# Kernel tuning notes

Measured on AMD Instinct MI355X. Metric: run time of the kernel, lower is better.

## Reference

```python
import jax, jax.numpy as jnp
import numpy as np

N_HOPS = 2
DIM = 64
N_REL = 17          # n_relations; groups G = N_REL - 1 = 16
N_MEM = 32
BATCH = 1024
N_ENT = 100000      # entity table has N_ENT + 1 rows
KGE_W = 0.01
L2_W = 1e-5


def setup_inputs() -> dict:
    key = jax.random.key(0)
    ks = jax.random.split(key, 10)
    G = N_REL - 1
    pos_items = jax.random.randint(ks[0], (BATCH,), 0, N_ENT + 1)
    neg_items = jax.random.randint(ks[1], (BATCH,), 0, N_ENT + 1)
    memories_h = jax.random.randint(ks[2], (N_HOPS, BATCH, G, N_MEM), 0, N_ENT + 1)
    memories_r = jax.random.randint(ks[3], (N_HOPS, BATCH, G, N_MEM), 0, N_REL)
    memories_t = jax.random.randint(ks[4], (N_HOPS, BATCH, G, N_MEM), 0, N_ENT + 1)
    # xavier-ish scales
    entity_emb = jax.random.normal(ks[5], (N_ENT + 1, DIM), jnp.float32) * 0.1
    relation_emb = jax.random.normal(ks[6], (N_REL, DIM), jnp.float32) * 0.1
    transform_matrix = jax.random.normal(ks[7], (DIM, DIM), jnp.float32) * 0.2
    attn_w1 = jax.random.normal(ks[8], (N_HOPS, DIM, DIM), jnp.float32) * 0.2
    attn_w2 = jax.random.normal(ks[9], (N_HOPS, DIM), jnp.float32) * 0.2
    return dict(pos_items=pos_items, neg_items=neg_items,
                memories_h=memories_h, memories_r=memories_r, memories_t=memories_t,
                entity_emb=entity_emb, relation_emb=relation_emb,
                transform_matrix=transform_matrix, attn_w1=attn_w1, attn_w2=attn_w2)


def reference(pos_items, neg_items, memories_h, memories_r, memories_t,
              entity_emb, relation_emb, transform_matrix, attn_w1, attn_w2):
    G = N_REL - 1
    items_emb = entity_emb[pos_items]          # [B, D] (v, fixed across hops as in source)
    neg_emb = entity_emb[neg_items]            # [B, D]

    o_list = []
    items_emb_new = items_emb
    kge = jnp.float32(0.0)
    l2 = jnp.float32(0.0)
    for hop in range(N_HOPS):
        h = entity_emb[memories_h[hop]]        # [B, G, M, D]
        r = relation_emb[memories_r[hop]]      # [B, G, M, D]
        t = entity_emb[memories_t[hop]]        # [B, G, M, D]

        # Rh @ v with Rh = h r^T collapses to h * (r . v)  (identical math, no [D,D] tensors)
        rv = jnp.einsum('bgmd,bd->bgm', r, items_emb)           # [B, G, M]
        probs = (h * rv[..., None]).reshape(-1, N_MEM)          # faithful row-major reshape (mixes m,d as in source)
        probs = jax.nn.softmax(probs, axis=-1)
        probs = probs.reshape(BATCH * G, N_MEM, DIM)
        o = jnp.sum(t.reshape(BATCH * G, N_MEM, DIM) * probs, axis=1)  # [B*G, D]
        o = o.reshape(BATCH, G, DIM)

        # attention layer: Linear(D,D) -> Dropout(eval: identity) -> Linear(D,1) -> ReLU
        hid = jnp.einsum('bgd,de->bge', o, attn_w1[hop])
        a = jax.nn.relu(jnp.einsum('bge,e->bg', hid, attn_w2[hop]))
        w = jax.nn.softmax(a, axis=-1)                          # [B, G]
        o_h = jnp.sum(o * w[..., None], axis=1)                 # [B, D]

        items_emb_new = (items_emb + o_h) @ transform_matrix    # note: v stays the ORIGINAL items_emb
        o_list.append(o_h)

        # kge: hRt = h * (r . t), then mean(sigmoid(.))
        rt = jnp.einsum('bgmd,bgmd->bgm', r, t)
        kge = kge + jnp.mean(jax.nn.sigmoid(h * rt[..., None]))
        # l2: mean(sum(x*x)) over whole tensor == sum(x*x)
        l2 = l2 + jnp.sum(h * h) + jnp.sum(t * t) + jnp.sum(r * r)

    y = o_list[0]
    for i in range(1, N_HOPS):
        y = y + o_list[i]
    scores = jnp.sum(items_emb_new * y, axis=-1)
    neg_scores = jnp.sum(neg_emb * y, axis=-1)
    mf_loss = -jnp.mean(jax.nn.log_sigmoid(scores - neg_scores))
    return mf_loss - KGE_W * kge + L2_W * l2
```

## Files before the change

### kernel.cpp

```cpp
#include <hip/hip_runtime.h>


#define BATCH 1024
#define G     16
#define NMEM  32
#define DIM   64
#define NREL  17

template<int CTRL>
__device__ __forceinline__ float dpp_add(float x) {
    int y = __builtin_amdgcn_update_dpp(0, __float_as_int(x), CTRL, 0xF, 0xF, true);
    return x + __int_as_float(y);
}
template<int OFF>
__device__ __forceinline__ float swz_add(float x) {
    int y = __builtin_amdgcn_ds_swizzle(__float_as_int(x), OFF);
    return x + __int_as_float(y);
}
__device__ __forceinline__ float bperm(int byteidx, float x) {
    return __int_as_float(__builtin_amdgcn_ds_bpermute(byteidx, __float_as_int(x)));
}
__device__ __forceinline__ float red32(float v) {
    v = dpp_add<0xB1>(v);
    v = dpp_add<0x4E>(v);
    v = dpp_add<0x124>(v);
    v = dpp_add<0x128>(v);
    v = swz_add<0x401F>(v);
    return v;
}

__global__ void kgan_prep(const float* __restrict__ attn_w1,
                          const float* __restrict__ attn_w2,
                          float* __restrict__ u, double* __restrict__ acc) {
    int t = threadIdx.x;
    if (t < 4) acc[t] = 0.0;
    int hop = t >> 6, d = t & 63;
    float s = 0.f;
#pragma unroll
    for (int e = 0; e < DIM; ++e)
        s = fmaf(attn_w1[(hop * DIM + d) * DIM + e], attn_w2[hop * DIM + e], s);
    u[t] = s;
}

__launch_bounds__(1024, 8)
__global__ void kgan_main(const int* __restrict__ pos_items,
                          const int* __restrict__ neg_items,
                          const int* __restrict__ mem_h,
                          const int* __restrict__ mem_r,
                          const int* __restrict__ mem_t,
                          const float* __restrict__ ent,
                          const float* __restrict__ rel,
                          const float* __restrict__ Tm,
                          const float* __restrict__ u,
                          double* __restrict__ acc) {
    const int b    = blockIdx.x;
    const int tid  = threadIdx.x;
    const int lane = tid & 63;
    const int g    = tid >> 6;
    const int gU   = __builtin_amdgcn_readfirstlane(g);
    const int x32  = (lane ^ 32) << 2;

    __shared__ float  rel_lds[NREL][DIM];
    __shared__ float2 rv_rs[NREL];
    __shared__ float  a_lds[G];
    __shared__ float  o_lds[G][DIM];
    __shared__ float  red_k[G];
    __shared__ float  red_l[G];
    __shared__ float  y_lds[DIM];

    for (int i = tid; i < NREL * DIM; i += 1024)
        ((float*)rel_lds)[i] = rel[i];
    const float v = ent[(size_t)pos_items[b] * DIM + lane];
    __syncthreads();

    for (int rr = gU; rr < NREL; rr += G) {
        float rd = rel_lds[rr][lane];
        float s1 = red32(rd * v); s1 += bperm(x32, s1);
        float s2 = red32(rd * rd); s2 += bperm(x32, s2);
        if (lane == 0) rv_rs[rr] = make_float2(s1, s2);
    }
    __syncthreads();

    float kge_acc = 0.f, l2_acc = 0.f, l2r_acc = 0.f;
    float y0 = 0.f;
    float x1 = 0.f;

    for (int hop = 0; hop < 2; ++hop) {
        const int base = ((hop * BATCH + b) * G + gU) * NMEM;
        float o_d = 0.f;
#pragma unroll 4
        for (int m = 0; m < NMEM; ++m) {
            const int ih = mem_h[base + m];
            const int it = mem_t[base + m];
            const int ir = mem_r[base + m];
            const float  h   = ent[(size_t)ih * DIM + lane];
            const float  t   = ent[(size_t)it * DIM + lane];
            const float  r   = rel_lds[ir][lane];
            const float2 rr2 = rv_rs[ir];

            float e = __expf(h * rr2.x);
            float p = r * t;
            float de = e, dp = p;
            de = dpp_add<0xB1>(de);   dp = dpp_add<0xB1>(dp);
            de = dpp_add<0x4E>(de);   dp = dpp_add<0x4E>(dp);
            de = dpp_add<0x124>(de);  dp = dpp_add<0x124>(dp);
            de = dpp_add<0x128>(de);  dp = dpp_add<0x128>(dp);
            de = swz_add<0x401F>(de); dp = swz_add<0x401F>(dp);
            const float rt = dp + bperm(x32, dp);

            o_d = fmaf(t, e * __builtin_amdgcn_rcpf(de), o_d);

            const float z = h * rt;
            kge_acc += __builtin_amdgcn_rcpf(1.f + __expf(-z));

            l2_acc  = fmaf(h, h, l2_acc);
            l2_acc  = fmaf(t, t, l2_acc);
            l2r_acc += rr2.y;
        }

        float a = red32(o_d * u[hop * DIM + lane]);
        a += bperm(x32, a);
        a = fmaxf(a, 0.f);
        if (lane == 0) a_lds[g] = a;
        o_lds[g][lane] = o_d;
        __syncthreads();

        if (g == 0) {
            float amax = -1e30f;
#pragma unroll
            for (int gg = 0; gg < G; ++gg) amax = fmaxf(amax, a_lds[gg]);
            float wexp[G]; float wsum = 0.f;
#pragma unroll
            for (int gg = 0; gg < G; ++gg) { wexp[gg] = __expf(a_lds[gg] - amax); wsum += wexp[gg]; }
            float inv = 1.f / wsum;
            float oh = 0.f;
#pragma unroll
            for (int gg = 0; gg < G; ++gg) oh = fmaf(o_lds[gg][lane], wexp[gg] * inv, oh);
            y0 += oh;
            if (hop == 1) x1 = v + oh;
        }
        __syncthreads();
    }

    float kk = red32(kge_acc); kk += bperm(x32, kk);
    float ll = red32(l2_acc);  ll += bperm(x32, ll);
    if (lane == 0) { red_k[g] = kk; red_l[g] = ll + l2r_acc; }
    if (g == 0) y_lds[lane] = y0;
    __syncthreads();

    if (tid == 0) {
        float sk = 0.f, sl = 0.f;
#pragma unroll
        for (int gg = 0; gg < G; ++gg) { sk += red_k[gg]; sl += red_l[gg]; }
        atomicAdd(&acc[1], (double)sk);
        atomicAdd(&acc[2], (double)sl);
    }

    if (g == 0) {
        float z = 0.f;
#pragma unroll
        for (int e = 0; e < DIM; ++e) z = fmaf(Tm[lane * DIM + e], y_lds[e], z);
        float score = red32(x1 * z);  score  += bperm(x32, score);
        float nv    = ent[(size_t)neg_items[b] * DIM + lane];
        float nsc   = red32(nv * y0); nsc    += bperm(x32, nsc);
        if (lane == 0) {
            float diff = score - nsc;
            float ls = fminf(diff, 0.f) - log1pf(__expf(-fabsf(diff)));
            atomicAdd(&acc[0], (double)ls);
        }
    }
}

__global__ void kgan_finalize(const double* __restrict__ acc, float* __restrict__ out) {
    double mf  = -acc[0] / (double)BATCH;
    double kge = acc[1] / ((double)BATCH * G * NMEM * DIM);
    double l2  = acc[2];
    out[0] = (float)(mf - 0.01 * kge + 1e-5 * l2);
}

extern "C" void kernel_launch(void* const* d_in, const int* in_sizes, int n_in,
                              void* d_out, int out_size, void* d_ws, size_t ws_size,
                              hipStream_t stream) {
    const int*   pos_items = (const int*)d_in[0];
    const int*   neg_items = (const int*)d_in[1];
    const int*   mem_h     = (const int*)d_in[2];
    const int*   mem_r     = (const int*)d_in[3];
    const int*   mem_t     = (const int*)d_in[4];
    const float* ent       = (const float*)d_in[5];
    const float* rel       = (const float*)d_in[6];
    const float* Tm        = (const float*)d_in[7];
    const float* attn_w1   = (const float*)d_in[8];
    const float* attn_w2   = (const float*)d_in[9];

    double* acc = (double*)d_ws;
    float*  u   = (float*)((char*)d_ws + 64);

    kgan_prep<<<1, 128, 0, stream>>>(attn_w1, attn_w2, u, acc);
    kgan_main<<<BATCH, 1024, 0, stream>>>(pos_items, neg_items, mem_h, mem_r, mem_t,
                                          ent, rel, Tm, u, acc);
    kgan_finalize<<<1, 1, 0, stream>>>(acc, (float*)d_out);
}
```

Measured before the change: 162.8 us.

## Process two groups per wave with software-prefetched gathers and permlane-swap reductions

Halves the block to 512 threads so each wave handles two relation groups. Index and entity-row loads are prefetched two memories ahead in double buffers to hide gather latency. Cross-lane reductions now use the gfx950 permlane16/permlane32 swap instructions instead of ds_swizzle and ds_bpermute, which avoids LDS-path traffic. The cost is higher register pressure from the prefetch buffers, which may reduce occupancy.

```diff
diff --git a/kernel.cpp b/kernel.cpp
--- a/kernel.cpp
+++ b/kernel.cpp
@@ -12,21 +12,20 @@
     int y = __builtin_amdgcn_update_dpp(0, __float_as_int(x), CTRL, 0xF, 0xF, true);
     return x + __int_as_float(y);
 }
-template<int OFF>
-__device__ __forceinline__ float swz_add(float x) {
-    int y = __builtin_amdgcn_ds_swizzle(__float_as_int(x), OFF);
-    return x + __int_as_float(y);
-}
-__device__ __forceinline__ float bperm(int byteidx, float x) {
-    return __int_as_float(__builtin_amdgcn_ds_bpermute(byteidx, __float_as_int(x)));
-}
-__device__ __forceinline__ float red32(float v) {
+__device__ __forceinline__ float red32p(float v) {
     v = dpp_add<0xB1>(v);
     v = dpp_add<0x4E>(v);
     v = dpp_add<0x124>(v);
     v = dpp_add<0x128>(v);
-    v = swz_add<0x401F>(v);
-    return v;
+    float a = v, b = v;
+    asm("v_permlane16_swap_b32 %0, %1" : "+v"(a), "+v"(b));
+    return a + b;
+}
+__device__ __forceinline__ float red64p(float v) {
+    v = red32p(v);
+    float a = v, b = v;
+    asm("v_permlane32_swap_b32 %0, %1" : "+v"(a), "+v"(b));
+    return a + b;
 }
 
 __global__ void kgan_prep(const float* __restrict__ attn_w1,
@@ -42,7 +41,38 @@
     u[t] = s;
 }
 
-__launch_bounds__(1024, 8)
+#define PREF(IH, IT, IR, HV, TV, M0)                                     \
+    _Pragma("unroll") for (int grp = 0; grp < 2; ++grp) {                \
+        _Pragma("unroll") for (int j = 0; j < 2; ++j) {                  \
+            IH[grp][j] = mem_h[base[grp] + (M0) + j];                    \
+            IT[grp][j] = mem_t[base[grp] + (M0) + j];                    \
+            IR[grp][j] = mem_r[base[grp] + (M0) + j];                    \
+            HV[grp][j] = ent[(size_t)IH[grp][j] * DIM + lane];           \
+            TV[grp][j] = ent[(size_t)IT[grp][j] * DIM + lane];           \
+        }                                                                \
+    }
+
+#define COMP(IR, HV, TV)                                                 \
+    _Pragma("unroll") for (int grp = 0; grp < 2; ++grp) {                \
+        _Pragma("unroll") for (int j = 0; j < 2; ++j) {                  \
+            const int    ir  = IR[grp][j];                               \
+            const float  h   = HV[grp][j];                               \
+            const float  t   = TV[grp][j];                               \
+            const float2 rr2 = rv_rs[ir];                                \
+            const float  r   = rel_lds[ir][lane];                        \
+            float e  = __expf(h * rr2.x);                                \
+            float de = red32p(e);                                        \
+            float rt = red64p(r * t);                                    \
+            o_d[grp] = fmaf(t, e * __builtin_amdgcn_rcpf(de), o_d[grp]); \
+            float z  = h * rt;                                           \
+            kge_acc += __builtin_amdgcn_rcpf(1.f + __expf(-z));          \
+            l2_acc   = fmaf(h, h, l2_acc);                               \
+            l2_acc   = fmaf(t, t, l2_acc);                               \
+            l2r_acc += rr2.y;                                            \
+        }                                                                \
+    }
+
+__launch_bounds__(512, 8)
 __global__ void kgan_main(const int* __restrict__ pos_items,
                           const int* __restrict__ neg_items,
                           const int* __restrict__ mem_h,
@@ -56,27 +86,27 @@
     const int b    = blockIdx.x;
     const int tid  = threadIdx.x;
     const int lane = tid & 63;
-    const int g    = tid >> 6;
-    const int gU   = __builtin_amdgcn_readfirstlane(g);
-    const int x32  = (lane ^ 32) << 2;
+    const int wid  = __builtin_amdgcn_readfirstlane(tid >> 6);
+    const int g0   = wid;
+    const int g1   = wid + 8;
 
     __shared__ float  rel_lds[NREL][DIM];
     __shared__ float2 rv_rs[NREL];
     __shared__ float  a_lds[G];
     __shared__ float  o_lds[G][DIM];
-    __shared__ float  red_k[G];
-    __shared__ float  red_l[G];
+    __shared__ float  red_k[8];
+    __shared__ float  red_l[8];
     __shared__ float  y_lds[DIM];
 
-    for (int i = tid; i < NREL * DIM; i += 1024)
+    for (int i = tid; i < NREL * DIM; i += 512)
         ((float*)rel_lds)[i] = rel[i];
     const float v = ent[(size_t)pos_items[b] * DIM + lane];
     __syncthreads();
 
-    for (int rr = gU; rr < NREL; rr += G) {
+    for (int rr = wid; rr < NREL; rr += 8) {
         float rd = rel_lds[rr][lane];
-        float s1 = red32(rd * v); s1 += bperm(x32, s1);
-        float s2 = red32(rd * rd); s2 += bperm(x32, s2);
+        float s1 = red64p(rd * v);
+        float s2 = red64p(rd * rd);
         if (lane == 0) rv_rs[rr] = make_float2(s1, s2);
     }
     __syncthreads();
@@ -85,47 +115,36 @@
     float y0 = 0.f;
     float x1 = 0.f;
 
+#pragma unroll 1
     for (int hop = 0; hop < 2; ++hop) {
-        const int base = ((hop * BATCH + b) * G + gU) * NMEM;
-        float o_d = 0.f;
-#pragma unroll 4
-        for (int m = 0; m < NMEM; ++m) {
-            const int ih = mem_h[base + m];
-            const int it = mem_t[base + m];
-            const int ir = mem_r[base + m];
-            const float  h   = ent[(size_t)ih * DIM + lane];
-            const float  t   = ent[(size_t)it * DIM + lane];
-            const float  r   = rel_lds[ir][lane];
-            const float2 rr2 = rv_rs[ir];
-
-            float e = __expf(h * rr2.x);
-            float p = r * t;
-            float de = e, dp = p;
-            de = dpp_add<0xB1>(de);   dp = dpp_add<0xB1>(dp);
-            de = dpp_add<0x4E>(de);   dp = dpp_add<0x4E>(dp);
-            de = dpp_add<0x124>(de);  dp = dpp_add<0x124>(dp);
-            de = dpp_add<0x128>(de);  dp = dpp_add<0x128>(dp);
-            de = swz_add<0x401F>(de); dp = swz_add<0x401F>(dp);
-            const float rt = dp + bperm(x32, dp);
-
-            o_d = fmaf(t, e * __builtin_amdgcn_rcpf(de), o_d);
-
-            const float z = h * rt;
-            kge_acc += __builtin_amdgcn_rcpf(1.f + __expf(-z));
-
-            l2_acc  = fmaf(h, h, l2_acc);
-            l2_acc  = fmaf(t, t, l2_acc);
-            l2r_acc += rr2.y;
+        int base[2];
+        base[0] = ((hop * BATCH + b) * G + g0) * NMEM;
+        base[1] = base[0] + 8 * NMEM;
+
+        float o_d[2] = {0.f, 0.f};
+        int   ih0[2][2], it0[2][2], ir0[2][2];
+        int   ih1[2][2], it1[2][2], ir1[2][2];
+        float hv0[2][2], tv0[2][2], hv1[2][2], tv1[2][2];
+
+        PREF(ih0, it0, ir0, hv0, tv0, 0);
+#pragma unroll 1
+        for (int mbp = 0; mbp < 8; ++mbp) {
+            const int m1 = mbp * 4 + 2;
+            PREF(ih1, it1, ir1, hv1, tv1, m1);
+            COMP(ir0, hv0, tv0);
+            if (mbp < 7) { PREF(ih0, it0, ir0, hv0, tv0, m1 + 2); }
+            COMP(ir1, hv1, tv1);
         }
 
-        float a = red32(o_d * u[hop * DIM + lane]);
-        a += bperm(x32, a);
-        a = fmaxf(a, 0.f);
-        if (lane == 0) a_lds[g] = a;
-        o_lds[g][lane] = o_d;
+        const float uh = u[hop * DIM + lane];
+        float a0 = fmaxf(red64p(o_d[0] * uh), 0.f);
+        float a1 = fmaxf(red64p(o_d[1] * uh), 0.f);
+        if (lane == 0) { a_lds[g0] = a0; a_lds[g1] = a1; }
+        o_lds[g0][lane] = o_d[0];
+        o_lds[g1][lane] = o_d[1];
         __syncthreads();
 
-        if (g == 0) {
+        if (wid == 0) {
             float amax = -1e30f;
 #pragma unroll
             for (int gg = 0; gg < G; ++gg) amax = fmaxf(amax, a_lds[gg]);
@@ -142,27 +161,27 @@
         __syncthreads();
     }
 
-    float kk = red32(kge_acc); kk += bperm(x32, kk);
-    float ll = red32(l2_acc);  ll += bperm(x32, ll);
-    if (lane == 0) { red_k[g] = kk; red_l[g] = ll + l2r_acc; }
-    if (g == 0) y_lds[lane] = y0;
+    float kk = red64p(kge_acc);
+    float ll = red64p(l2_acc);
+    if (lane == 0) { red_k[wid] = kk; red_l[wid] = ll + l2r_acc; }
+    if (wid == 0) y_lds[lane] = y0;
     __syncthreads();
 
     if (tid == 0) {
         float sk = 0.f, sl = 0.f;
 #pragma unroll
-        for (int gg = 0; gg < G; ++gg) { sk += red_k[gg]; sl += red_l[gg]; }
+        for (int gg = 0; gg < 8; ++gg) { sk += red_k[gg]; sl += red_l[gg]; }
         atomicAdd(&acc[1], (double)sk);
         atomicAdd(&acc[2], (double)sl);
     }
 
-    if (g == 0) {
+    if (wid == 0) {
         float z = 0.f;
 #pragma unroll
         for (int e = 0; e < DIM; ++e) z = fmaf(Tm[lane * DIM + e], y_lds[e], z);
-        float score = red32(x1 * z);  score  += bperm(x32, score);
+        float score = red64p(x1 * z);
         float nv    = ent[(size_t)neg_items[b] * DIM + lane];
-        float nsc   = red32(nv * y0); nsc    += bperm(x32, nsc);
+        float nsc   = red64p(nv * y0);
         if (lane == 0) {
             float diff = score - nsc;
             float ls = fminf(diff, 0.f) - log1pf(__expf(-fabsf(diff)));
@@ -196,7 +215,7 @@
     float*  u   = (float*)((char*)d_ws + 64);
 
     kgan_prep<<<1, 128, 0, stream>>>(attn_w1, attn_w2, u, acc);
-    kgan_main<<<BATCH, 1024, 0, stream>>>(pos_items, neg_items, mem_h, mem_r, mem_t,
-                                          ent, rel, Tm, u, acc);
+    kgan_main<<<BATCH, 512, 0, stream>>>(pos_items, neg_items, mem_h, mem_r, mem_t,
+                                         ent, rel, Tm, u, acc);
     kgan_finalize<<<1, 1, 0, stream>>>(acc, (float*)d_out);
 }
```

Result: slower. 193.2 us (+18.7%).
